# Kernel tuning notes

Measured on AMD Instinct MI355X. Metric: run time of the kernel, lower is better.

Reference implementation:

```python
import jax, jax.numpy as jnp
import numpy as np
from jax import lax

BSZ, BEAM, VOCAB, D = 32, 4, 50257, 1024
MAXLEN = 64
L = MAXLEN + 2            # tokens buffer length (bos + maxlen+1 slots)
SLEN = MAXLEN + 1         # scores buffer length
PAD, EOS, UNK = 1, 2, 3
TEMP = 1.0
LEN_PEN = 1.0
UNK_PEN = 0.0
NEG = jnp.float32(-1e9)   # stand-in for -inf (safe for grads)


def setup_inputs() -> dict:
    key = jax.random.key(0)
    k1, k2, k3 = jax.random.split(key, 3)
    # 0.02 scaling keeps logits in a realistic range
    emb = jax.random.normal(k1, (VOCAB, D), jnp.float32) * 0.02
    W_out = jax.random.normal(k2, (D, VOCAB), jnp.float32) * 0.02
    pos_emb = jax.random.normal(k3, (SLEN, D), jnp.float32) * 0.02
    return {"emb": emb, "W_out": W_out, "pos_emb": pos_emb}


def _decode(emb, W_out, pos_emb, tokens, step):
    # stand-in decoder: prev-token embedding + pos embedding -> vocab logits
    prev = lax.dynamic_index_in_dim(tokens, step, axis=1, keepdims=False)  # [bbsz]
    h = emb[prev] + pos_emb[step]                                          # [bbsz, D]
    lp = jax.nn.log_softmax((h @ W_out) / TEMP, axis=-1)                   # [bbsz, V]
    lp = lp.at[:, PAD].set(NEG)
    lp = lp.at[:, UNK].add(-UNK_PEN)
    return lp


def _beam_search(emb, W_out, pos_emb):
    bbsz = BSZ * BEAM
    tokens = jnp.full((bbsz, L), PAD, jnp.int32).at[:, 0].set(EOS)
    scores = jnp.zeros((bbsz, SLEN), jnp.float32)
    fin_tok = jnp.zeros((BSZ, BEAM, L), jnp.int32)
    fin_sc = jnp.full((BSZ, BEAM), NEG, jnp.float32)
    offsets = jnp.arange(2 * BEAM, dtype=jnp.int32)
    colL = jnp.arange(L)
    colS = jnp.arange(SLEN)
    barange = jnp.arange(BEAM)

    def step_fn(carry, step):
        tokens, scores, fin_tok, fin_sc = carry
        lp = _decode(emb, W_out, pos_emb, tokens, step).reshape(BSZ, BEAM, VOCAB)
        prev_sc = lax.dynamic_index_in_dim(scores, jnp.maximum(step - 1, 0), axis=1, keepdims=False)
        prev_sc = jnp.where(step == 0, 0.0, prev_sc).reshape(BSZ, BEAM)
        cum = lp + prev_sc[:, :, None]
        # step 0: only the first beam participates (fairseq BeamSearch.step)
        cum = jnp.where((step == 0) & (barange[None, :, None] > 0), NEG, cum)
        cand_sc, cand_flat = lax.top_k(cum.reshape(BSZ, BEAM * VOCAB), 2 * BEAM)
        cand_beam = cand_flat // VOCAB       # [BSZ, 2*BEAM]
        cand_tok = cand_flat % VOCAB
        tokens3 = tokens.reshape(BSZ, BEAM, L)
        # --- finalize eos hypotheses from the first BEAM candidates ---
        eos_mask_b = cand_tok[:, :BEAM] == EOS
        eos_norm = jnp.where(eos_mask_b, cand_sc[:, :BEAM] / (step + 1.0) ** LEN_PEN, NEG)
        eos_tok = jnp.take_along_axis(tokens3, cand_beam[:, :BEAM, None], axis=1)
        eos_tok = jnp.where(colL[None, None, :] == step + 1, EOS, eos_tok)
        all_sc = jnp.concatenate([fin_sc, eos_norm], axis=1)
        all_tok = jnp.concatenate([fin_tok, eos_tok], axis=1)
        fin_sc, sel = lax.top_k(all_sc, BEAM)
        fin_tok = jnp.take_along_axis(all_tok, sel[:, :, None], axis=1)
        # --- pick BEAM active (non-eos) hypotheses (smallest active_mask) ---
        eos_mask = (cand_tok == EOS).astype(jnp.int32)
        amask = eos_mask * (2 * BEAM) + offsets[None, :]
        _, active = lax.top_k(-amask, BEAM)
        act_beam = jnp.take_along_axis(cand_beam, active, axis=1)
        act_tok = jnp.take_along_axis(cand_tok, active, axis=1)
        act_sc = jnp.take_along_axis(cand_sc, active, axis=1)
        # --- reorder beams, append new token / score ---
        tokens3 = jnp.take_along_axis(tokens3, act_beam[:, :, None], axis=1)
        tokens3 = jnp.where(colL[None, None, :] == step + 1, act_tok[:, :, None], tokens3)
        scores3 = jnp.take_along_axis(scores.reshape(BSZ, BEAM, SLEN), act_beam[:, :, None], axis=1)
        scores3 = jnp.where(colS[None, None, :] == step, act_sc[:, :, None], scores3)
        return (tokens3.reshape(bbsz, L), scores3.reshape(bbsz, SLEN), fin_tok, fin_sc), None

    carry = (tokens, scores, fin_tok, fin_sc)
    (tokens, scores, fin_tok, fin_sc), _ = lax.scan(step_fn, carry, jnp.arange(MAXLEN))
    # --- final step: force EOS on every surviving beam (step == maxlen) ---
    lp = _decode(emb, W_out, pos_emb, tokens, MAXLEN)
    eos_sc = (scores[:, MAXLEN - 1] + lp[:, EOS]).reshape(BSZ, BEAM) / (MAXLEN + 1.0) ** LEN_PEN
    tokens3 = tokens.reshape(BSZ, BEAM, L)
    eos_tok = jnp.where(jnp.arange(L)[None, None, :] == MAXLEN + 1, EOS, tokens3)
    all_sc = jnp.concatenate([fin_sc, eos_sc], axis=1)
    all_tok = jnp.concatenate([fin_tok, eos_tok], axis=1)
    fin_sc, sel = lax.top_k(all_sc, BEAM)
    fin_tok = jnp.take_along_axis(all_tok, sel[:, :, None], axis=1)
    return fin_tok, fin_sc


def reference(emb, W_out, pos_emb):
    # returns (finalized tokens [BSZ, BEAM, L] int32, normalized scores [BSZ, BEAM] f32)
    return _beam_search(emb, W_out, pos_emb)
```

## Files before the change

### kernel.cpp

```cpp
#include <hip/hip_runtime.h>
#include <cstdint>
#include <cstddef>

#define VOCAB_N 50257
#define NPAD    50304
#define DIM     1024
#define BSZ_N   32
#define BEAM_N  4
#define BB      128
#define L_N     66
#define SLEN_N  65
#define MAXLEN_N 64
#define PAD_T   1
#define EOS_T   2
#define NEGV    (-1e9f)
#define SENTV   (-3.402823466e38f)
#define PW_BLOCK 128
#define HSPLIT  25128

typedef unsigned long long u64;
typedef __attribute__((ext_vector_type(8))) _Float16 f16x8;
typedef __attribute__((ext_vector_type(4))) _Float16 f16x4;
typedef __attribute__((ext_vector_type(4))) float f32x4;

struct PWTree {
    int nleaf, nint, maxlev, root;
    int lstart[512], lnum[512], lslot[512];
    int eL[512], eR[512], eD[512];
    int lvl[32];
};

constexpr PWTree build_tree(int start, int n0) {
    PWTree t{};
    int fs[64] = {}, fn[64] = {}, fstt[64] = {}, fls[64] = {}, fll[64] = {};
    int tL[512] = {}, tR[512] = {}, tD[512] = {}, tLev[512] = {};
    int sp = 0, lc = 0, nc = 0, cnt = 0;
    fs[0] = start; fn[0] = n0; fstt[0] = 0; sp = 1;
    int retslot = -1, retlev = 0;
    while (sp > 0) {
        const int n = fn[sp - 1], s = fs[sp - 1], st = fstt[sp - 1];
        if (n <= PW_BLOCK) {
            t.lstart[lc] = s; t.lnum[lc] = n; t.lslot[lc] = cnt;
            retslot = cnt; retlev = 0; ++cnt; ++lc; --sp; continue;
        }
        int L = (n >> 1); L -= (L & 7);
        if (st == 0)      { fstt[sp - 1] = 1; fs[sp] = s;     fn[sp] = L;     fstt[sp] = 0; ++sp; }
        else if (st == 1) { fls[sp - 1] = retslot; fll[sp - 1] = retlev; fstt[sp - 1] = 2;
                            fs[sp] = s + L; fn[sp] = n - L; fstt[sp] = 0; ++sp; }
        else {
            const int lv = (fll[sp - 1] > retlev ? fll[sp - 1] : retlev) + 1;
            tL[nc] = fls[sp - 1]; tR[nc] = retslot; tD[nc] = cnt; tLev[nc] = lv;
            retslot = cnt; retlev = lv; ++cnt; ++nc; --sp;
        }
    }
    int maxlev = 0;
    for (int j = 0; j < nc; ++j) if (tLev[j] > maxlev) maxlev = tLev[j];
    int cl[40] = {};
    for (int j = 0; j < nc; ++j) cl[tLev[j]]++;
    int acc = 0;
    for (int v = 1; v <= maxlev; ++v) { t.lvl[v] = acc; acc += cl[v]; }
    t.lvl[maxlev + 1] = acc;
    int pos[40] = {};
    for (int v = 1; v <= maxlev; ++v) pos[v] = t.lvl[v];
    for (int j = 0; j < nc; ++j) {
        const int v = tLev[j]; const int p = pos[v]++;
        t.eL[p] = tL[j]; t.eR[p] = tR[j]; t.eD[p] = tD[j];
    }
    t.nleaf = lc; t.nint = nc; t.maxlev = maxlev; t.root = retslot;
    return t;
}

__device__ constexpr PWTree g_treeL = build_tree(0, HSPLIT);
__device__ constexpr PWTree g_treeR = build_tree(HSPLIT, VOCAB_N - HSPLIT);

__device__ __forceinline__ unsigned sortable_f32(float x) {
    unsigned u = __float_as_uint(x);
    return (u & 0x80000000u) ? ~u : (u | 0x80000000u);
}
__device__ __forceinline__ float unsort_f32(unsigned s) {
    unsigned u = (s & 0x80000000u) ? (s & 0x7fffffffu) : ~s;
    return __uint_as_float(u);
}

__global__ void k_init(int* __restrict__ tokens, float* __restrict__ scores,
                       int* __restrict__ fin_tok, float* __restrict__ fin_sc,
                       unsigned* __restrict__ rmax_u) {
    int i = blockIdx.x * blockDim.x + threadIdx.x;
    int st = gridDim.x * blockDim.x;
    for (int k = i; k < BB * L_N; k += st) tokens[k] = ((k % L_N) == 0) ? EOS_T : PAD_T;
    for (int k = i; k < BB * SLEN_N; k += st) scores[k] = 0.f;
    for (int k = i; k < BB * L_N; k += st) fin_tok[k] = 0;
    for (int k = i; k < BB; k += st) { fin_sc[k] = NEGV; rmax_u[k] = 0u; }
}

__device__ __forceinline__ void split2(float x, _Float16& h0, _Float16& h1) {
    const float xs = x * 4096.f;
    h0 = (_Float16)xs;
    const float r = xs - (float)h0;
    h1 = (_Float16)r;
}

#define KT 32
__global__ __launch_bounds__(512) void k_gemm(const float* __restrict__ W,
                                              const float* __restrict__ emb,
                                              const float* __restrict__ pos_emb,
                                              const int* __restrict__ tokens,
                                              float* __restrict__ logits,
                                              unsigned* __restrict__ rmax_u, int step) {
    __shared__ __align__(16) _Float16 Ha[2][128][40];
    __shared__ __align__(16) _Float16 Wb[2][128][40];
    __shared__ unsigned smax[128];
    const int tid = threadIdx.x;
    const int n0 = blockIdx.x * 128;
    const bool full = (n0 + 128 <= VOCAB_N);

    const int lane = tid & 63, wid = tid >> 6;
    const int wr = wid >> 1;
    const int wc = wid & 1;
    const int la = lane & 15, g = lane >> 4;

    const int hrow = tid & 127;
    const int hkq  = tid >> 7;
    const int tokH = tokens[hrow * L_N + step];
    const float* eprow = emb + (size_t)tokH * DIM;
    const float* pprow = pos_emb + (size_t)step * DIM;
    const int wcq = tid & 31;
    const int wk  = tid >> 5;

    if (tid < 128) smax[tid] = 0u;

    f32x4 acc[2][4];
#pragma unroll
    for (int mf = 0; mf < 2; ++mf)
#pragma unroll
        for (int nf = 0; nf < 4; ++nf)
#pragma unroll
            for (int j = 0; j < 4; ++j) acc[mf][nf][j] = 0.f;

    for (int k0 = 0; k0 < DIM; k0 += KT) {
#pragma unroll
        for (int d = 0; d < 4; ++d) {
            const int c = wcq + 32 * d;
#pragma unroll
            for (int qq = 0; qq < 2; ++qq) {
                const int kk = wk + 16 * qq;
                float wv = 0.f;
                if (full || (n0 + c < VOCAB_N))
                    wv = W[(size_t)(k0 + kk) * VOCAB_N + n0 + c];
                _Float16 b0, b1;
                split2(wv, b0, b1);
                Wb[0][c][kk] = b0;
                Wb[1][c][kk] = b1;
            }
        }
#pragma unroll
        for (int qq = 0; qq < 2; ++qq) {
            const int kq = hkq + 4 * qq;
            const float4 e0 = *(const float4*)(eprow + k0 + kq * 4);
            const float4 p0 = *(const float4*)(pprow + k0 + kq * 4);
            const float hv[4] = {e0.x + p0.x, e0.y + p0.y, e0.z + p0.z, e0.w + p0.w};
            f16x4 o0, o1;
#pragma unroll
            for (int d = 0; d < 4; ++d) {
                _Float16 a0, a1;
                split2(hv[d], a0, a1);
                o0[d] = a0; o1[d] = a1;
            }
            *(f16x4*)&Ha[0][hrow][kq * 4] = o0;
            *(f16x4*)&Ha[1][hrow][kq * 4] = o1;
        }
        __syncthreads();

        f16x8 af[2][2];
#pragma unroll
        for (int mf = 0; mf < 2; ++mf)
#pragma unroll
            for (int p = 0; p < 2; ++p)
                af[mf][p] = *(const f16x8*)&Ha[p][wr * 32 + mf * 16 + la][g * 8];
#pragma unroll
        for (int nf = 0; nf < 4; ++nf) {
            const int c = wc * 64 + nf * 16 + la;
            const f16x8 b0 = *(const f16x8*)&Wb[0][c][g * 8];
            const f16x8 b1 = *(const f16x8*)&Wb[1][c][g * 8];
#pragma unroll
            for (int mf = 0; mf < 2; ++mf) {
                f32x4 cc = acc[mf][nf];
                cc = __builtin_amdgcn_mfma_f32_16x16x32_f16(af[mf][0], b0, cc, 0, 0, 0);
                cc = __builtin_amdgcn_mfma_f32_16x16x32_f16(af[mf][0], b1, cc, 0, 0, 0);
                cc = __builtin_amdgcn_mfma_f32_16x16x32_f16(af[mf][1], b0, cc, 0, 0, 0);
                acc[mf][nf] = cc;
            }
        }
        __syncthreads();
    }

#pragma unroll
    for (int mf = 0; mf < 2; ++mf) {
        const int row = wr * 32 + mf * 16 + g * 4;
        float rmx[4] = {SENTV, SENTV, SENTV, SENTV};
#pragma unroll
        for (int nf = 0; nf < 4; ++nf) {
            const int col = n0 + wc * 64 + nf * 16 + la;
#pragma unroll
            for (int j = 0; j < 4; ++j) {
                const float v = acc[mf][nf][j] * 0x1p-24f;
                logits[(size_t)(row + j) * NPAD + col] = v;
                rmx[j] = fmaxf(rmx[j], v);
            }
        }
#pragma unroll
        for (int j = 0; j < 4; ++j) {
            float v = rmx[j];
            v = fmaxf(v, __shfl_xor(v, 1, 64));
            v = fmaxf(v, __shfl_xor(v, 2, 64));
            v = fmaxf(v, __shfl_xor(v, 4, 64));
            v = fmaxf(v, __shfl_xor(v, 8, 64));
            if (la == 0) atomicMax(&smax[row + j], sortable_f32(v));
        }
    }
    __syncthreads();
    if (tid < 128) atomicMax(&rmax_u[tid], smax[tid]);
}

__device__ __forceinline__ u64 pack_key(float x, int tk) {
    return ((u64)sortable_f32(x) << 32) | (unsigned)(VOCAB_N - tk);
}
__device__ __forceinline__ void insk16(u64 k, u64 lst[16]) {
#pragma unroll
    for (int p = 0; p < 16; ++p) {
        if (k > lst[p]) { u64 o = lst[p]; lst[p] = k; k = o; }
    }
}
__device__ __forceinline__ u64 wave_max_u64(u64 v) {
#pragma unroll
    for (int o = 32; o > 0; o >>= 1) {
        u64 w = __shfl_xor(v, o, 64);
        if (w > v) v = w;
    }
    return v;
}

#define RT_THR 512
__global__ __launch_bounds__(RT_THR) void k_scanexp(const float* __restrict__ logits,
                                                    const unsigned* __restrict__ rmax_u,
                                                    u64* __restrict__ htop,
                                                    float* __restrict__ halfsum) {
    const int hb = blockIdx.x;
    const int row = hb >> 1, half = hb & 1;
    const int tid = threadIdx.x;
    const int lane = tid & 63, wid = tid >> 6;
    const float* x = logits + (size_t)row * NPAD;
    const int lo = half ? HSPLIT : 0;
    const int hi = half ? VOCAB_N : HSPLIT;
    const float mrow = unsort_f32(rmax_u[row]);

    u64 lst[16];
#pragma unroll
    for (int p = 0; p < 16; ++p) lst[p] = 0ULL;
    for (int v = lo + tid * 4; v + 3 < hi; v += RT_THR * 4) {
        const float4 t = *(const float4*)(x + v);
        const float va[4] = {t.x, t.y, t.z, t.w};
#pragma unroll
        for (int u = 0; u < 4; ++u) {
            const int tk = v + u;
            if (tk == PAD_T) continue;
            const u64 key = pack_key(va[u], tk);
            if (key > lst[15]) insk16(key, lst);
        }
    }
    if (half == 1 && tid == 0) {
        const int tk = VOCAB_N - 1;
        const u64 key = pack_key(x[tk], tk);
        if (key > lst[15]) insk16(key, lst);
    }

    __shared__ u64 wtop[8][16];
    for (int pass = 0; pass < 16; ++pass) {
        const u64 cand = lst[0];
        const u64 mx = wave_max_u64(cand);
        const u64 ball = __ballot(cand == mx);
        const int first = __ffsll((u64)ball) - 1;
        if (lane == first) {
#pragma unroll
            for (int p = 0; p < 15; ++p) lst[p] = lst[p + 1];
            lst[15] = 0ULL;
        }
        if (lane == 0) wtop[wid][pass] = mx;
    }
    __syncthreads();

    __shared__ u64 sfin[16];
    if (tid < 64) {
        u64 a = wtop[tid >> 3][(tid & 7) * 2];
        u64 b = wtop[tid >> 3][(tid & 7) * 2 + 1];
        for (int pass = 0; pass < 16; ++pass) {
            const u64 mx = wave_max_u64(a);
            const u64 ball = __ballot(a == mx);
            const int first = __ffsll((u64)ball) - 1;
            if (tid == first) { a = b; b = 0ULL; }
            if (tid == 0) sfin[pass] = mx;
        }
    }

    const PWTree& T = half ? g_treeR : g_treeL;
    __shared__ float slot[1024];
    for (int leaf = tid; leaf < T.nleaf; leaf += RT_THR) {
        const int s = T.lstart[leaf];
        const int n = T.lnum[leaf];
        float res;
        if (n < 8) {
            res = 0.f;
            for (int i = 0; i < n; ++i) res += expf(x[s + i] - mrow);
        } else {
            float r0 = expf(x[s + 0] - mrow), r1 = expf(x[s + 1] - mrow);
            float r2 = expf(x[s + 2] - mrow), r3 = expf(x[s + 3] - mrow);
            float r4 = expf(x[s + 4] - mrow), r5 = expf(x[s + 5] - mrow);
            float r6 = expf(x[s + 6] - mrow), r7 = expf(x[s + 7] - mrow);
            int i = 8;
            const int lim = n - (n & 7);
            for (; i < lim; i += 8) {
                r0 += expf(x[s + i + 0] - mrow); r1 += expf(x[s + i + 1] - mrow);
                r2 += expf(x[s + i + 2] - mrow); r3 += expf(x[s + i + 3] - mrow);
                r4 += expf(x[s + i + 4] - mrow); r5 += expf(x[s + i + 5] - mrow);
                r6 += expf(x[s + i + 6] - mrow); r7 += expf(x[s + i + 7] - mrow);
            }
            res = ((r0 + r1) + (r2 + r3)) + ((r4 + r5) + (r6 + r7));
            for (; i < n; ++i) res += expf(x[s + i] - mrow);
        }
        slot[T.lslot[leaf]] = res;
    }
    __syncthreads();
    for (int lev = 1; lev <= T.maxlev; ++lev) {
        for (int j = T.lvl[lev] + tid; j < T.lvl[lev + 1]; j += RT_THR)
            slot[T.eD[j]] = slot[T.eL[j]] + slot[T.eR[j]];
        __syncthreads();
    }
    if (tid == 0) halfsum[hb] = slot[T.root];
    if (tid < 16) htop[hb * 16 + tid] = sfin[tid];
}

__global__ __launch_bounds__(256) void k_beam(const u64* __restrict__ htop,
                                              unsigned* __restrict__ rmax_u,
                                              const float* __restrict__ halfsum,
                                              int* __restrict__ tokens,
                                              float* __restrict__ scores,
                                              int* __restrict__ fin_tok,
                                              float* __restrict__ fin_sc,
                                              int step) {
    const int sent = blockIdx.x;
    const int tid = threadIdx.x;
    const int rN = (step == 0) ? 1 : BEAM_N;

    __shared__ u64 keys[4][32];
    for (int e = tid; e < 128; e += 256) {
        const int r = e >> 5, i = e & 31;
        keys[r][i] = htop[((sent * BEAM_N + r) * 2 + (i >> 4)) * 16 + (i & 15)];
    }
    __syncthreads();

    __shared__ u64 merged[4][16];
    if (tid < 4) {
        int ia = 0, ib = 0;
        for (int o = 0; o < 16; ++o) {
            const u64 a = (ia < 16) ? keys[tid][ia] : 0ULL;
            const u64 b = (ib < 16) ? keys[tid][16 + ib] : 0ULL;
            const bool ta = a > b;
            merged[tid][o] = ta ? a : b;
            ia += ta ? 1 : 0; ib += ta ? 0 : 1;
        }
    }
    __syncthreads();

    __shared__ float bval[64]; __shared__ int bflat[64];
    if (tid < 16 * rN) {
        const int r = tid >> 4, j = tid & 15;
        const int row = sent * BEAM_N + r;
        const float rm = unsort_f32(rmax_u[row]);
        const float rl = (float)log((double)(halfsum[row * 2] + halfsum[row * 2 + 1]));
        const float prev = (step == 0) ? 0.f : scores[row * SLEN_N + step - 1];
        const u64 k = merged[r][j];
        const float xv = unsort_f32((unsigned)(k >> 32));
        const int   tk = VOCAB_N - (int)(k & 0xFFFFFFFFu);
        bval[tid]  = ((xv - rm) - rl) + prev;
        bflat[tid] = r * VOCAB_N + tk;
    }
    __syncthreads();
    __shared__ float cand_sc[8]; __shared__ int cand_flat[8];
    if (tid == 0) {
        const int nC = 16 * rN;
        for (int pass = 0; pass < 8; ++pass) {
            float bv = SENTV; int bi = 0x7fffffff; int bs = -1;
            for (int k = 0; k < nC; ++k) {
                const float v = bval[k]; const int ix = bflat[k];
                if (v > bv || (v == bv && ix < bi)) { bv = v; bi = ix; bs = k; }
            }
            cand_sc[pass] = bv; cand_flat[pass] = bi;
            bval[bs] = SENTV; bflat[bs] = 0x7fffffff;
        }
    }
    __syncthreads();

    __shared__ int   cur_tok[BEAM_N * L_N];
    __shared__ int   cur_fin[BEAM_N * L_N];
    __shared__ float cur_sc[BEAM_N * SLEN_N];
    for (int e = tid; e < BEAM_N * L_N; e += 256) {
        cur_tok[e] = tokens[sent * (BEAM_N * L_N) + e];
        cur_fin[e] = fin_tok[sent * (BEAM_N * L_N) + e];
    }
    for (int e = tid; e < BEAM_N * SLEN_N; e += 256)
        cur_sc[e] = scores[sent * (BEAM_N * SLEN_N) + e];
    __syncthreads();

    __shared__ int   tmp_fin[BEAM_N * L_N];
    __shared__ int   tmp_tok[BEAM_N * L_N];
    __shared__ float tmp_sc[BEAM_N * SLEN_N];
    __shared__ float nfin_s[BEAM_N];
    if (tid == 0) {
        int cb[8], ct[8];
#pragma unroll
        for (int j = 0; j < 8; ++j) {
            cb[j] = cand_flat[j] / VOCAB_N;
            ct[j] = cand_flat[j] % VOCAB_N;
        }
        float allsc[8];
#pragma unroll
        for (int j = 0; j < 4; ++j) allsc[j] = fin_sc[sent * BEAM_N + j];
#pragma unroll
        for (int j = 0; j < 4; ++j)
            allsc[4 + j] = (ct[j] == EOS_T) ? (cand_sc[j] / (float)(step + 1)) : NEGV;
        int fsel[4]; float nfin[4];
        bool used[8] = {false,false,false,false,false,false,false,false};
#pragma unroll
        for (int b = 0; b < 4; ++b) {
            int best = -1; float bvv = 0.f;
#pragma unroll
            for (int j = 0; j < 8; ++j) {
                if (used[j]) continue;
                if (best < 0 || allsc[j] > bvv) { best = j; bvv = allsc[j]; }
            }
            used[best] = true; fsel[b] = best; nfin[b] = bvv;
        }
#pragma unroll
        for (int b = 0; b < 4; ++b) {
            const int s = fsel[b];
            if (s < 4) {
                for (int p = 0; p < L_N; ++p) tmp_fin[b * L_N + p] = cur_fin[s * L_N + p];
            } else {
                const int bm = cb[s - 4];
                for (int p = 0; p < L_N; ++p)
                    tmp_fin[b * L_N + p] = (p == step + 1) ? EOS_T : cur_tok[bm * L_N + p];
            }
        }
        int ab[4], atk[4]; float asc[4]; int na = 0;
#pragma unroll
        for (int j = 0; j < 8; ++j) {
            if (na < 4 && ct[j] != EOS_T) { ab[na] = cb[j]; atk[na] = ct[j]; asc[na] = cand_sc[j]; ++na; }
        }
#pragma unroll
        for (int b = 0; b < 4; ++b) {
            const int bm = ab[b];
            for (int p = 0; p < L_N; ++p)
                tmp_tok[b * L_N + p] = (p == step + 1) ? atk[b] : cur_tok[bm * L_N + p];
            for (int p = 0; p < SLEN_N; ++p)
                tmp_sc[b * SLEN_N + p] = (p == step) ? asc[b] : cur_sc[bm * SLEN_N + p];
        }
#pragma unroll
        for (int b = 0; b < 4; ++b) nfin_s[b] = nfin[b];
    }
    __syncthreads();

    for (int e = tid; e < BEAM_N * L_N; e += 256) {
        fin_tok[sent * (BEAM_N * L_N) + e] = tmp_fin[e];
        tokens[sent * (BEAM_N * L_N) + e]  = tmp_tok[e];
    }
    for (int e = tid; e < BEAM_N * SLEN_N; e += 256)
        scores[sent * (BEAM_N * SLEN_N) + e] = tmp_sc[e];
    if (tid < 4) {
        fin_sc[sent * BEAM_N + tid] = nfin_s[tid];
        rmax_u[sent * BEAM_N + tid] = 0u;
    }
}

__global__ __launch_bounds__(256) void k_final(const float* __restrict__ logits,
                                               const unsigned* __restrict__ rmax_u,
                                               const float* __restrict__ halfsum,
                                               const int* __restrict__ tokens,
                                               const float* __restrict__ scores,
                                               const int* __restrict__ fin_tok,
                                               const float* __restrict__ fin_sc,
                                               float* __restrict__ out) {
    const int sent = blockIdx.x;
    const int tid = threadIdx.x;
    __shared__ int fsel_s[4]; __shared__ float nfin_s[4];
    if (tid == 0) {
        float allsc[8];
#pragma unroll
        for (int r = 0; r < 4; ++r) {
            const int row = sent * BEAM_N + r;
            const float rm = unsort_f32(rmax_u[row]);
            const float rl = (float)log((double)(halfsum[row * 2] + halfsum[row * 2 + 1]));
            const float lpE = ((logits[(size_t)row * NPAD + EOS_T] - rm) - rl);
            allsc[r] = fin_sc[sent * BEAM_N + r];
            allsc[4 + r] = (scores[row * SLEN_N + (MAXLEN_N - 1)] + lpE) / 65.0f;
        }
        bool used[8] = {false,false,false,false,false,false,false,false};
#pragma unroll
        for (int b = 0; b < 4; ++b) {
            int best = -1; float bvv = 0.f;
#pragma unroll
            for (int j = 0; j < 8; ++j) {
                if (used[j]) continue;
                if (best < 0 || allsc[j] > bvv) { best = j; bvv = allsc[j]; }
            }
            used[best] = true; fsel_s[b] = best; nfin_s[b] = bvv;
        }
    }
    __syncthreads();
    for (int e = tid; e < BEAM_N * L_N; e += 256) {
        const int b = e / L_N, p = e % L_N;
        const int s = fsel_s[b]; int valt;
        if (s < 4) {
            valt = fin_tok[(sent * BEAM_N + s) * L_N + p];
        } else {
            const int r = s - 4;
            valt = (p == MAXLEN_N + 1) ? EOS_T : tokens[(sent * BEAM_N + r) * L_N + p];
        }
        out[(size_t)(sent * BEAM_N + b) * L_N + p] = (float)valt;
    }
    if (tid < 4) out[BSZ_N * BEAM_N * L_N + sent * BEAM_N + tid] = nfin_s[tid];
}

extern "C" void kernel_launch(void* const* d_in, const int* in_sizes, int n_in,
                              void* d_out, int out_size, void* d_ws, size_t ws_size,
                              hipStream_t stream) {
    const float* emb = (const float*)d_in[0];
    const float* W   = (const float*)d_in[1];
    const float* pos = (const float*)d_in[2];
    float* out = (float*)d_out;

    char* w = (char*)d_ws;
    float*    logits  = (float*)w;    w += (size_t)BB * NPAD * 4;
    unsigned* rmax_u  = (unsigned*)w; w += BB * 4;
    float*    halfsum = (float*)w;    w += BB * 2 * 4;
    u64*      htop    = (u64*)w;      w += (size_t)BB * 2 * 16 * 8;
    int*      tokens  = (int*)w;      w += BB * L_N * 4;
    float*    scores  = (float*)w;    w += BB * SLEN_N * 4;
    int*      ftok    = (int*)w;      w += BB * L_N * 4;
    float*    fsc     = (float*)w;    w += BB * 4;

    k_init<<<32, 256, 0, stream>>>(tokens, scores, ftok, fsc, rmax_u);
    for (int s = 0; s < MAXLEN_N; ++s) {
        k_gemm<<<NPAD / 128, 512, 0, stream>>>(W, emb, pos, tokens, logits, rmax_u, s);
        k_scanexp<<<BB * 2, RT_THR, 0, stream>>>(logits, rmax_u, htop, halfsum);
        k_beam<<<BSZ_N, 256, 0, stream>>>(htop, rmax_u, halfsum, tokens, scores, ftok, fsc, s);
    }
    k_gemm<<<NPAD / 128, 512, 0, stream>>>(W, emb, pos, tokens, logits, rmax_u, MAXLEN_N);
    k_scanexp<<<BB * 2, RT_THR, 0, stream>>>(logits, rmax_u, htop, halfsum);
    k_final<<<BSZ_N, 256, 0, stream>>>(logits, rmax_u, halfsum, tokens, scores, ftok, fsc, out);
}
```

Before: 13.95 ms.

## Pre-split W to fp16 pair once, stream it in GEMM; quarter vocab scan

Adds a one-time kernel that converts W_out into a transposed, K-contiguous fp16 hi/lo pair layout, plus a per-step kernel that builds the split hidden states. The per-step GEMM then streams prepacked fp16 data with register prefetch instead of reloading fp32 W and re-splitting it every one of the 65 steps. The top-k/exp-sum scan is also split into four vocab quarters with 256-thread blocks for more parallelism, and the beam merge now combines four lists. This costs about 200MB of extra workspace and an upfront conversion pass, and falls back to the old path if the workspace is too small.

```diff
diff --git a/kernel.cpp b/kernel.cpp
--- a/kernel.cpp
+++ b/kernel.cpp
@@ -16,24 +16,26 @@
 #define NEGV    (-1e9f)
 #define SENTV   (-3.402823466e38f)
 #define PW_BLOCK 128
-#define HSPLIT  25128
 
 typedef unsigned long long u64;
 typedef __attribute__((ext_vector_type(8))) _Float16 f16x8;
 typedef __attribute__((ext_vector_type(4))) _Float16 f16x4;
 typedef __attribute__((ext_vector_type(4))) float f32x4;
 
+__device__ __constant__ int QLO[4] = {0, 12560, 25128, 37688};
+__device__ __constant__ int QHI[4] = {12560, 25128, 37688, 50257};
+
 struct PWTree {
     int nleaf, nint, maxlev, root;
-    int lstart[512], lnum[512], lslot[512];
-    int eL[512], eR[512], eD[512];
+    int lstart[256], lnum[256], lslot[256];
+    int eL[256], eR[256], eD[256];
     int lvl[32];
 };
 
 constexpr PWTree build_tree(int start, int n0) {
     PWTree t{};
     int fs[64] = {}, fn[64] = {}, fstt[64] = {}, fls[64] = {}, fll[64] = {};
-    int tL[512] = {}, tR[512] = {}, tD[512] = {}, tLev[512] = {};
+    int tL[256] = {}, tR[256] = {}, tD[256] = {}, tLev[256] = {};
     int sp = 0, lc = 0, nc = 0, cnt = 0;
     fs[0] = start; fn[0] = n0; fstt[0] = 0; sp = 1;
     int retslot = -1, retlev = 0;
@@ -70,8 +72,10 @@
     return t;
 }
 
-__device__ constexpr PWTree g_treeL = build_tree(0, HSPLIT);
-__device__ constexpr PWTree g_treeR = build_tree(HSPLIT, VOCAB_N - HSPLIT);
+__device__ constexpr PWTree g_q0 = build_tree(0, 12560);
+__device__ constexpr PWTree g_q1 = build_tree(12560, 12568);
+__device__ constexpr PWTree g_q2 = build_tree(25128, 12560);
+__device__ constexpr PWTree g_q3 = build_tree(37688, 12569);
 
 __device__ __forceinline__ unsigned sortable_f32(float x) {
     unsigned u = __float_as_uint(x);
@@ -100,32 +104,173 @@
     h1 = (_Float16)r;
 }
 
+__global__ __launch_bounds__(256) void k_wsplit(const float* __restrict__ W,
+                                                _Float16* __restrict__ Wsp) {
+    __shared__ __align__(16) _Float16 B[2][64][40];
+    const int bid = blockIdx.x;
+    const int ct = bid % 786, kt = bid / 786;
+    const int n0 = ct * 64, k0 = kt * 32;
+    const int tid = threadIdx.x;
+    const int c = tid & 63, kk = tid >> 6;
+#pragma unroll
+    for (int j = 0; j < 8; ++j) {
+        const int k = kk * 8 + j;
+        float wv = 0.f;
+        if (n0 + c < VOCAB_N) wv = W[(size_t)(k0 + k) * VOCAB_N + n0 + c];
+        _Float16 b0, b1;
+        split2(wv, b0, b1);
+        B[0][c][k] = b0; B[1][c][k] = b1;
+    }
+    __syncthreads();
+    const int g = tid & 3, cc = (tid >> 2) & 63;
+#pragma unroll
+    for (int p = 0; p < 2; ++p)
+        *(f16x8*)&Wsp[((size_t)p * NPAD + n0 + cc) * 1024 + k0 + g * 8] =
+            *(const f16x8*)&B[p][cc][g * 8];
+}
+
+__global__ __launch_bounds__(256) void k_hsplit(const float* __restrict__ emb,
+                                                const float* __restrict__ pos_emb,
+                                                const int* __restrict__ tokens,
+                                                _Float16* __restrict__ Hsp, int step) {
+    const int row = blockIdx.x;
+    const int tid = threadIdx.x;
+    const int tok = tokens[row * L_N + step];
+    const float4 e = *(const float4*)(emb + (size_t)tok * DIM + tid * 4);
+    const float4 p = *(const float4*)(pos_emb + (size_t)step * DIM + tid * 4);
+    const float hv[4] = {e.x + p.x, e.y + p.y, e.z + p.z, e.w + p.w};
+    f16x4 o0, o1;
+#pragma unroll
+    for (int d = 0; d < 4; ++d) {
+        _Float16 a0, a1;
+        split2(hv[d], a0, a1);
+        o0[d] = a0; o1[d] = a1;
+    }
+    *(f16x4*)&Hsp[(size_t)0 * 131072 + row * 1024 + tid * 4] = o0;
+    *(f16x4*)&Hsp[(size_t)1 * 131072 + row * 1024 + tid * 4] = o1;
+}
+
+__global__ __launch_bounds__(512) void k_gemm_fast(const _Float16* __restrict__ Wsp,
+                                                   const _Float16* __restrict__ Hsp,
+                                                   float* __restrict__ logits,
+                                                   unsigned* __restrict__ rmax_u) {
+    __shared__ __align__(16) _Float16 Ha[2][128][40];
+    __shared__ __align__(16) _Float16 Wb[2][128][40];
+    __shared__ unsigned smax[128];
+    const int tid = threadIdx.x;
+    const int n0 = blockIdx.x * 128;
+    const int lane = tid & 63, wid = tid >> 6;
+    const int la = lane & 15, g = lane >> 4;
+    const int wr = wid >> 1, wc = wid & 1;
+    const int sg = tid & 3, sidx = (tid >> 2) & 127;
+
+    if (tid < 128) smax[tid] = 0u;
+
+    f32x4 acc[2][4];
+#pragma unroll
+    for (int mf = 0; mf < 2; ++mf)
+#pragma unroll
+        for (int nf = 0; nf < 4; ++nf)
+#pragma unroll
+            for (int j = 0; j < 4; ++j) acc[mf][nf][j] = 0.f;
+
+    const _Float16* H0 = Hsp;
+    const _Float16* H1 = Hsp + 131072;
+    const _Float16* W0 = Wsp;
+    const _Float16* W1 = Wsp + (size_t)NPAD * 1024;
+    const size_t hoff = (size_t)sidx * 1024 + sg * 8;
+    const size_t woff = (size_t)(n0 + sidx) * 1024 + sg * 8;
+
+    f16x8 rH0 = *(const f16x8*)&H0[hoff];
+    f16x8 rH1 = *(const f16x8*)&H1[hoff];
+    f16x8 rW0 = *(const f16x8*)&W0[woff];
+    f16x8 rW1 = *(const f16x8*)&W1[woff];
+
+    for (int t = 0; t < 32; ++t) {
+        *(f16x8*)&Ha[0][sidx][sg * 8] = rH0;
+        *(f16x8*)&Ha[1][sidx][sg * 8] = rH1;
+        *(f16x8*)&Wb[0][sidx][sg * 8] = rW0;
+        *(f16x8*)&Wb[1][sidx][sg * 8] = rW1;
+        __syncthreads();
+        if (t + 1 < 32) {
+            const int k0 = (t + 1) * 32;
+            rH0 = *(const f16x8*)&H0[hoff + k0];
+            rH1 = *(const f16x8*)&H1[hoff + k0];
+            rW0 = *(const f16x8*)&W0[woff + k0];
+            rW1 = *(const f16x8*)&W1[woff + k0];
+        }
+        f16x8 a[2][2];
+#pragma unroll
+        for (int mf = 0; mf < 2; ++mf) {
+            a[mf][0] = *(const f16x8*)&Ha[0][wr * 32 + mf * 16 + la][g * 8];
+            a[mf][1] = *(const f16x8*)&Ha[1][wr * 32 + mf * 16 + la][g * 8];
+        }
+#pragma unroll
+        for (int nf = 0; nf < 4; ++nf) {
+            const int c = wc * 64 + nf * 16 + la;
+            const f16x8 b0 = *(const f16x8*)&Wb[0][c][g * 8];
+            const f16x8 b1 = *(const f16x8*)&Wb[1][c][g * 8];
+#pragma unroll
+            for (int mf = 0; mf < 2; ++mf) {
+                f32x4 cc = acc[mf][nf];
+                cc = __builtin_amdgcn_mfma_f32_16x16x32_f16(a[mf][0], b0, cc, 0, 0, 0);
+                cc = __builtin_amdgcn_mfma_f32_16x16x32_f16(a[mf][0], b1, cc, 0, 0, 0);
+                cc = __builtin_amdgcn_mfma_f32_16x16x32_f16(a[mf][1], b0, cc, 0, 0, 0);
+                acc[mf][nf] = cc;
+            }
+        }
+        __syncthreads();
+    }
+
+#pragma unroll
+    for (int mf = 0; mf < 2; ++mf) {
+        const int row = wr * 32 + mf * 16 + g * 4;
+        float rmx[4] = {SENTV, SENTV, SENTV, SENTV};
+#pragma unroll
+        for (int nf = 0; nf < 4; ++nf) {
+            const int col = n0 + wc * 64 + nf * 16 + la;
+#pragma unroll
+            for (int j = 0; j < 4; ++j) {
+                const float v = acc[mf][nf][j] * 0x1p-24f;
+                logits[(size_t)(row + j) * NPAD + col] = v;
+                rmx[j] = fmaxf(rmx[j], v);
+            }
+        }
+#pragma unroll
+        for (int j = 0; j < 4; ++j) {
+            float v = rmx[j];
+            v = fmaxf(v, __shfl_xor(v, 1, 64));
+            v = fmaxf(v, __shfl_xor(v, 2, 64));
+            v = fmaxf(v, __shfl_xor(v, 4, 64));
+            v = fmaxf(v, __shfl_xor(v, 8, 64));
+            if (la == 0) atomicMax(&smax[row + j], sortable_f32(v));
+        }
+    }
+    __syncthreads();
+    if (tid < 128) atomicMax(&rmax_u[tid], smax[tid]);
+}
+
 #define KT 32
-__global__ __launch_bounds__(512) void k_gemm(const float* __restrict__ W,
-                                              const float* __restrict__ emb,
-                                              const float* __restrict__ pos_emb,
-                                              const int* __restrict__ tokens,
-                                              float* __restrict__ logits,
-                                              unsigned* __restrict__ rmax_u, int step) {
+__global__ __launch_bounds__(512) void k_gemm_slow(const float* __restrict__ W,
+                                                   const float* __restrict__ emb,
+                                                   const float* __restrict__ pos_emb,
+                                                   const int* __restrict__ tokens,
+                                                   float* __restrict__ logits,
+                                                   unsigned* __restrict__ rmax_u, int step) {
     __shared__ __align__(16) _Float16 Ha[2][128][40];
     __shared__ __align__(16) _Float16 Wb[2][128][40];
     __shared__ unsigned smax[128];
     const int tid = threadIdx.x;
     const int n0 = blockIdx.x * 128;
     const bool full = (n0 + 128 <= VOCAB_N);
-
     const int lane = tid & 63, wid = tid >> 6;
-    const int wr = wid >> 1;
-    const int wc = wid & 1;
+    const int wr = wid >> 1, wc = wid & 1;
     const int la = lane & 15, g = lane >> 4;
-
-    const int hrow = tid & 127;
-    const int hkq  = tid >> 7;
+    const int hrow = tid & 127, hkq = tid >> 7;
     const int tokH = tokens[hrow * L_N + step];
     const float* eprow = emb + (size_t)tokH * DIM;
     const float* pprow = pos_emb + (size_t)step * DIM;
-    const int wcq = tid & 31;
-    const int wk  = tid >> 5;
+    const int wcq = tid & 31, wk = tid >> 5;
 
     if (tid < 128) smax[tid] = 0u;
 
@@ -170,7 +315,6 @@
             *(f16x4*)&Ha[1][hrow][kq * 4] = o1;
         }
         __syncthreads();
-
         f16x8 af[2][2];
 #pragma unroll
         for (int mf = 0; mf < 2; ++mf)
@@ -193,7 +337,6 @@
         }
         __syncthreads();
     }
-
 #pragma unroll
     for (int mf = 0; mf < 2; ++mf) {
         const int row = wr * 32 + mf * 16 + g * 4;
@@ -240,24 +383,23 @@
     return v;
 }
 
-#define RT_THR 512
-__global__ __launch_bounds__(RT_THR) void k_scanexp(const float* __restrict__ logits,
-                                                    const unsigned* __restrict__ rmax_u,
-                                                    u64* __restrict__ htop,
-                                                    float* __restrict__ halfsum) {
+#define RT2 256
+__global__ __launch_bounds__(RT2) void k_scanexp(const float* __restrict__ logits,
+                                                 const unsigned* __restrict__ rmax_u,
+                                                 u64* __restrict__ htop,
+                                                 float* __restrict__ qsum) {
     const int hb = blockIdx.x;
-    const int row = hb >> 1, half = hb & 1;
+    const int row = hb >> 2, q = hb & 3;
     const int tid = threadIdx.x;
     const int lane = tid & 63, wid = tid >> 6;
     const float* x = logits + (size_t)row * NPAD;
-    const int lo = half ? HSPLIT : 0;
-    const int hi = half ? VOCAB_N : HSPLIT;
+    const int lo = QLO[q], hi = QHI[q];
     const float mrow = unsort_f32(rmax_u[row]);
 
     u64 lst[16];
 #pragma unroll
     for (int p = 0; p < 16; ++p) lst[p] = 0ULL;
-    for (int v = lo + tid * 4; v + 3 < hi; v += RT_THR * 4) {
+    for (int v = lo + tid * 4; v + 3 < hi; v += RT2 * 4) {
         const float4 t = *(const float4*)(x + v);
         const float va[4] = {t.x, t.y, t.z, t.w};
 #pragma unroll
@@ -268,13 +410,13 @@
             if (key > lst[15]) insk16(key, lst);
         }
     }
-    if (half == 1 && tid == 0) {
+    if (q == 3 && tid == 0) {
         const int tk = VOCAB_N - 1;
         const u64 key = pack_key(x[tk], tk);
         if (key > lst[15]) insk16(key, lst);
     }
 
-    __shared__ u64 wtop[8][16];
+    __shared__ u64 wtop[4][16];
     for (int pass = 0; pass < 16; ++pass) {
         const u64 cand = lst[0];
         const u64 mx = wave_max_u64(cand);
@@ -291,20 +433,21 @@
 
     __shared__ u64 sfin[16];
     if (tid < 64) {
-        u64 a = wtop[tid >> 3][(tid & 7) * 2];
-        u64 b = wtop[tid >> 3][(tid & 7) * 2 + 1];
+        const u64 mine = wtop[tid >> 4][tid & 15];
+        bool taken = false;
         for (int pass = 0; pass < 16; ++pass) {
-            const u64 mx = wave_max_u64(a);
-            const u64 ball = __ballot(a == mx);
+            const u64 cand = taken ? 0ULL : mine;
+            const u64 mx = wave_max_u64(cand);
+            const u64 ball = __ballot(cand == mx);
             const int first = __ffsll((u64)ball) - 1;
-            if (tid == first) { a = b; b = 0ULL; }
+            if (tid == first) taken = true;
             if (tid == 0) sfin[pass] = mx;
         }
     }
 
-    const PWTree& T = half ? g_treeR : g_treeL;
-    __shared__ float slot[1024];
-    for (int leaf = tid; leaf < T.nleaf; leaf += RT_THR) {
+    const PWTree& T = (q == 0) ? g_q0 : (q == 1) ? g_q1 : (q == 2) ? g_q2 : g_q3;
+    __shared__ float slot[512];
+    for (int leaf = tid; leaf < T.nleaf; leaf += RT2) {
         const int s = T.lstart[leaf];
         const int n = T.lnum[leaf];
         float res;
@@ -331,17 +474,17 @@
     }
     __syncthreads();
     for (int lev = 1; lev <= T.maxlev; ++lev) {
-        for (int j = T.lvl[lev] + tid; j < T.lvl[lev + 1]; j += RT_THR)
+        for (int j = T.lvl[lev] + tid; j < T.lvl[lev + 1]; j += RT2)
             slot[T.eD[j]] = slot[T.eL[j]] + slot[T.eR[j]];
         __syncthreads();
     }
-    if (tid == 0) halfsum[hb] = slot[T.root];
+    if (tid == 0) qsum[hb] = slot[T.root];
     if (tid < 16) htop[hb * 16 + tid] = sfin[tid];
 }
 
 __global__ __launch_bounds__(256) void k_beam(const u64* __restrict__ htop,
                                               unsigned* __restrict__ rmax_u,
-                                              const float* __restrict__ halfsum,
+                                              const float* __restrict__ qsum,
                                               int* __restrict__ tokens,
                                               float* __restrict__ scores,
                                               int* __restrict__ fin_tok,
@@ -351,22 +494,24 @@
     const int tid = threadIdx.x;
     const int rN = (step == 0) ? 1 : BEAM_N;
 
-    __shared__ u64 keys[4][32];
-    for (int e = tid; e < 128; e += 256) {
-        const int r = e >> 5, i = e & 31;
-        keys[r][i] = htop[((sent * BEAM_N + r) * 2 + (i >> 4)) * 16 + (i & 15)];
+    __shared__ u64 keys[4][64];
+    for (int e = tid; e < 256; e += 256) {
+        const int r = e >> 6, i = e & 63;
+        keys[r][i] = htop[((sent * BEAM_N + r) * 4 + (i >> 4)) * 16 + (i & 15)];
     }
     __syncthreads();
 
     __shared__ u64 merged[4][16];
     if (tid < 4) {
-        int ia = 0, ib = 0;
+        int ia[4] = {0, 0, 0, 0};
         for (int o = 0; o < 16; ++o) {
-            const u64 a = (ia < 16) ? keys[tid][ia] : 0ULL;
-            const u64 b = (ib < 16) ? keys[tid][16 + ib] : 0ULL;
-            const bool ta = a > b;
-            merged[tid][o] = ta ? a : b;
-            ia += ta ? 1 : 0; ib += ta ? 0 : 1;
+            u64 best = 0ULL; int bq = 0;
+#pragma unroll
+            for (int qq = 0; qq < 4; ++qq) {
+                const u64 h = (ia[qq] < 16) ? keys[tid][qq * 16 + ia[qq]] : 0ULL;
+                if (h > best) { best = h; bq = qq; }
+            }
+            merged[tid][o] = best; ia[bq]++;
         }
     }
     __syncthreads();
@@ -376,7 +521,8 @@
         const int r = tid >> 4, j = tid & 15;
         const int row = sent * BEAM_N + r;
         const float rm = unsort_f32(rmax_u[row]);
-        const float rl = (float)log((double)(halfsum[row * 2] + halfsum[row * 2 + 1]));
+        const float rl = (float)log((double)((qsum[row * 4] + qsum[row * 4 + 1]) +
+                                             (qsum[row * 4 + 2] + qsum[row * 4 + 3])));
         const float prev = (step == 0) ? 0.f : scores[row * SLEN_N + step - 1];
         const u64 k = merged[r][j];
         const float xv = unsort_f32((unsigned)(k >> 32));
@@ -483,7 +629,7 @@
 
 __global__ __launch_bounds__(256) void k_final(const float* __restrict__ logits,
                                                const unsigned* __restrict__ rmax_u,
-                                               const float* __restrict__ halfsum,
+                                               const float* __restrict__ qsum,
                                                const int* __restrict__ tokens,
                                                const float* __restrict__ scores,
                                                const int* __restrict__ fin_tok,
@@ -498,7 +644,8 @@
         for (int r = 0; r < 4; ++r) {
             const int row = sent * BEAM_N + r;
             const float rm = unsort_f32(rmax_u[row]);
-            const float rl = (float)log((double)(halfsum[row * 2] + halfsum[row * 2 + 1]));
+            const float rl = (float)log((double)((qsum[row * 4] + qsum[row * 4 + 1]) +
+                                                 (qsum[row * 4 + 2] + qsum[row * 4 + 3])));
             const float lpE = ((logits[(size_t)row * NPAD + EOS_T] - rm) - rl);
             allsc[r] = fin_sc[sent * BEAM_N + r];
             allsc[4 + r] = (scores[row * SLEN_N + (MAXLEN_N - 1)] + lpE) / 65.0f;
@@ -539,22 +686,38 @@
     float* out = (float*)d_out;
 
     char* w = (char*)d_ws;
-    float*    logits  = (float*)w;    w += (size_t)BB * NPAD * 4;
-    unsigned* rmax_u  = (unsigned*)w; w += BB * 4;
-    float*    halfsum = (float*)w;    w += BB * 2 * 4;
-    u64*      htop    = (u64*)w;      w += (size_t)BB * 2 * 16 * 8;
-    int*      tokens  = (int*)w;      w += BB * L_N * 4;
-    float*    scores  = (float*)w;    w += BB * SLEN_N * 4;
-    int*      ftok    = (int*)w;      w += BB * L_N * 4;
-    float*    fsc     = (float*)w;    w += BB * 4;
+    size_t off = 0;
+    auto alloc = [&](size_t bytes) { void* p = w + off; off += (bytes + 15) & ~(size_t)15; return p; };
+    float*    logits = (float*)alloc((size_t)BB * NPAD * 4);
+    unsigned* rmax_u = (unsigned*)alloc(BB * 4);
+    float*    qsum   = (float*)alloc(BB * 4 * 4);
+    u64*      htop   = (u64*)alloc((size_t)BB * 4 * 16 * 8);
+    int*      tokens = (int*)alloc(BB * L_N * 4);
+    float*    scores = (float*)alloc(BB * SLEN_N * 4);
+    int*      ftok   = (int*)alloc(BB * L_N * 4);
+    float*    fsc    = (float*)alloc(BB * 4);
+    _Float16* Wsp    = (_Float16*)alloc((size_t)2 * NPAD * 1024 * 2);
+    _Float16* Hsp    = (_Float16*)alloc((size_t)2 * 128 * 1024 * 2);
+    const bool fast = (off <= ws_size);
 
     k_init<<<32, 256, 0, stream>>>(tokens, scores, ftok, fsc, rmax_u);
+    if (fast) k_wsplit<<<786 * 32, 256, 0, stream>>>(W, Wsp);
     for (int s = 0; s < MAXLEN_N; ++s) {
-        k_gemm<<<NPAD / 128, 512, 0, stream>>>(W, emb, pos, tokens, logits, rmax_u, s);
-        k_scanexp<<<BB * 2, RT_THR, 0, stream>>>(logits, rmax_u, htop, halfsum);
-        k_beam<<<BSZ_N, 256, 0, stream>>>(htop, rmax_u, halfsum, tokens, scores, ftok, fsc, s);
-    }
-    k_gemm<<<NPAD / 128, 512, 0, stream>>>(W, emb, pos, tokens, logits, rmax_u, MAXLEN_N);
-    k_scanexp<<<BB * 2, RT_THR, 0, stream>>>(logits, rmax_u, htop, halfsum);
-    k_final<<<BSZ_N, 256, 0, stream>>>(logits, rmax_u, halfsum, tokens, scores, ftok, fsc, out);
-}
+        if (fast) {
+            k_hsplit<<<128, 256, 0, stream>>>(emb, pos, tokens, Hsp, s);
+            k_gemm_fast<<<NPAD / 128, 512, 0, stream>>>(Wsp, Hsp, logits, rmax_u);
+        } else {
+            k_gemm_slow<<<NPAD / 128, 512, 0, stream>>>(W, emb, pos, tokens, logits, rmax_u, s);
+        }
+        k_scanexp<<<BB * 4, RT2, 0, stream>>>(logits, rmax_u, htop, qsum);
+        k_beam<<<BSZ_N, 256, 0, stream>>>(htop, rmax_u, qsum, tokens, scores, ftok, fsc, s);
+    }
+    if (fast) {
+        k_hsplit<<<128, 256, 0, stream>>>(emb, pos, tokens, Hsp, MAXLEN_N);
+        k_gemm_fast<<<NPAD / 128, 512, 0, stream>>>(Wsp, Hsp, logits, rmax_u);
+    } else {
+        k_gemm_slow<<<NPAD / 128, 512, 0, stream>>>(W, emb, pos, tokens, logits, rmax_u, MAXLEN_N);
+    }
+    k_scanexp<<<BB * 4, RT2, 0, stream>>>(logits, rmax_u, htop, qsum);
+    k_final<<<BSZ_N, 256, 0, stream>>>(logits, rmax_u, qsum, tokens, scores, ftok, fsc, out);
+}
```

After: 11.81 ms. 15.4% less time.
